# Performance work log

Hardware: AMD Instinct MI355X
Metric: run time of the kernel (lower is better)

Reference implementation:

```python
import jax, jax.numpy as jnp
import numpy as np

N_PTS, N_NODES, N_EDGES, N_CMP = 512, 10000, 50000, 64
# edge types produced by _get_edge_states, plus NULL (do_include_null=True, do_include_all_16=False)
EDGE_TYPES = jnp.array([0, 2, 3, 5, 9], dtype=jnp.int32)  # NULL, NOR, NCONV, NIMPL, AND
N_TYPES = 5
# mapping of temp = 2*a+b in {0,1,2,3} -> edge-type code
TEMP_TO_CODE = jnp.array([2, 3, 5, 9], dtype=jnp.int32)  # NOR, NCONV, NIMPL, AND


def _edge_to_logical(es):
    # es: (n, E) int codes -> (n, N_TYPES*E) bool, type-major layout matching
    # torch.permute([1,0,2]).reshape(n, n_types*n_edges)
    oh = es[:, None, :] == EDGE_TYPES[None, :, None]  # (n, N_TYPES, E)
    return oh.reshape(es.shape[0], N_TYPES * es.shape[1])


def setup_inputs() -> dict:
    key = jax.random.key(0)
    k1, k2, k3 = jax.random.split(key, 3)
    node_activations = jax.random.randint(k1, (N_PTS, N_NODES), 0, 2, dtype=jnp.int32)
    edge_endnode_idx = jax.random.randint(k2, (N_EDGES, 2), 0, N_NODES, dtype=jnp.int32)
    # learned edge states: random categorical over the 5 reachable types
    learned_type_idx = jax.random.randint(k3, (N_CMP, N_EDGES), 0, N_TYPES, dtype=jnp.int32)
    learned_codes = EDGE_TYPES[learned_type_idx]
    binarized_learned = _edge_to_logical(learned_codes).astype(jnp.float32)  # (N_CMP, 5*E)
    return {
        "node_activations": node_activations,
        "binarized_learned": binarized_learned,
        "edge_endnode_idx": edge_endnode_idx,
    }


def reference(node_activations, binarized_learned, edge_endnode_idx):
    # gather endpoint activations: (n_pts, n_edges)
    a = node_activations[:, edge_endnode_idx[:, 0]]
    b = node_activations[:, edge_endnode_idx[:, 1]]
    temp = 2 * a + b  # in {0,1,2,3}
    code = TEMP_TO_CODE[temp]  # edge_type_filter is empty -> no filtering
    # one-hot encode edge states: (n_pts, 5*n_edges)
    bact = _edge_to_logical(code).astype(binarized_learned.dtype)
    # energies: (n_pts, n_cmp); torch does int8 matmul of the same 0/1 values
    energies = jnp.einsum('ck,nk->nc', binarized_learned, bact)
    return energies - jnp.min(energies)
```

## Files before the change

kernel.cpp:

```cpp
#include <hip/hip_runtime.h>
#include <stdint.h>

#define N_PTS   512
#define N_NODES 10000
#define N_EDGES 50000
#define N_CMP   64
#define W64     784
#define EBITS   (W64 * 64)
#define LSTRIDE (N_CMP * W64)
#define NCHUNK  49
#define CW      16
#define TN      16
#define BST_ROW 10016
#define NB_BST  ((N_NODES + 255) / 256)
#define NBLK_L  (NCHUNK * N_CMP)

typedef unsigned long long u64;

__global__ void build_all(const int* __restrict__ act, const float* __restrict__ BL,
                          u64* __restrict__ Lp, uint16_t* __restrict__ bsT) {
    int bid = blockIdx.x;
    int t = threadIdx.x;
    if (bid < NBLK_L) {
        __shared__ uint16_t sh[256];
        int c = bid / NCHUNK, bx = bid % NCHUNK;
        int e0 = bx * 1024 + 4 * t;
        int nla = 0, nlb = 0, ntz = 0xF;
        if (e0 < N_EDGES) {
            const float* base = BL + (size_t)c * (5 * N_EDGES) + e0;
            float4 p0 = *(const float4*)(base);
            float4 p2 = *(const float4*)(base + 2 * N_EDGES);
            float4 p3 = *(const float4*)(base + 3 * N_EDGES);
            float4 p4 = *(const float4*)(base + 4 * N_EDGES);
            #define B_(f) ((f) != 0.f ? 1 : 0)
            nla = (B_(p3.x) | B_(p4.x)) | ((B_(p3.y) | B_(p4.y)) << 1)
                | ((B_(p3.z) | B_(p4.z)) << 2) | ((B_(p3.w) | B_(p4.w)) << 3);
            nlb = (B_(p2.x) | B_(p4.x)) | ((B_(p2.y) | B_(p4.y)) << 1)
                | ((B_(p2.z) | B_(p4.z)) << 2) | ((B_(p2.w) | B_(p4.w)) << 3);
            ntz = B_(p0.x) | (B_(p0.y) << 1) | (B_(p0.z) << 2) | (B_(p0.w) << 3);
            #undef B_
        }
        sh[t] = (uint16_t)(nla | (nlb << 4) | (ntz << 8));
        __syncthreads();
        if (t < 48) {
            int p = t >> 4, w = t & 15;
            const u64* v = (const u64*)sh + w * 4;
            u64 word = 0;
            #pragma unroll
            for (int i = 0; i < 4; ++i) {
                u64 x = v[i];
                #pragma unroll
                for (int kk = 0; kk < 4; ++kk)
                    word |= ((x >> (16 * kk + 4 * p)) & 0xFULL) << (4 * (i * 4 + kk));
            }
            Lp[(size_t)p * LSTRIDE + (size_t)c * W64 + bx * 16 + w] = word;
        }
    } else {
        int rem = bid - NBLK_L;
        int g = rem / NB_BST, nb = rem % NB_BST;
        int node = nb * 256 + t;
        if (node < N_NODES) {
            uint32_t m = 0;
            #pragma unroll
            for (int p = 0; p < TN; ++p)
                m |= (act[(size_t)(g * TN + p) * N_NODES + node] != 0 ? 1u : 0u) << p;
            bsT[(size_t)g * BST_ROW + node] = (uint16_t)m;
        }
    }
}

__global__ void __launch_bounds__(512, 6)
match_fused(const u64* __restrict__ Lp, const uint16_t* __restrict__ bsT,
            const int2* __restrict__ edges, uint32_t* __restrict__ part32) {
    __shared__ u64 Ll[3][CW][65];
    __shared__ uint16_t bsTl[BST_ROW];
    __shared__ int2 edgl[CW * 64];

    int chunk = blockIdx.x;
    int g = blockIdx.y;
    int t = threadIdx.x;
    int lane = t & 63;
    int wave = t >> 6;
    int cw0 = chunk * CW;

    {
        int w = t & 15;
        #pragma unroll
        for (int pass = 0; pass < 6; ++pass) {
            int r = pass * 32 + (t >> 4);
            int plane = r >> 6, c = r & 63;
            Ll[plane][w][c] = Lp[(size_t)plane * LSTRIDE + (size_t)c * W64 + cw0 + w];
        }
    }
    {
        const uint4* src = (const uint4*)(bsT + (size_t)g * BST_ROW);
        uint4* dst = (uint4*)bsTl;
        for (int idx = t; idx < BST_ROW / 8; idx += 512) dst[idx] = src[idx];
    }
    {
        int e = chunk * 1024 + t;
        edgl[t]       = edges[min(e, N_EDGES - 1)];
        edgl[t + 512] = edges[min(e + 512, N_EDGES - 1)];
    }
    __syncthreads();

    int cnt0 = 0, cnt1 = 0;
    #pragma unroll
    for (int w = 0; w < CW; ++w) {
        int2 cur = edgl[w * 64 + lane];
        uint32_t a16 = bsTl[cur.x];
        uint32_t b16 = bsTl[cur.y];
        u64 A0 = __ballot((a16 >> wave) & 1);
        u64 B0 = __ballot((b16 >> wave) & 1);
        u64 A1 = __ballot((a16 >> (wave + 8)) & 1);
        u64 B1 = __ballot((b16 >> (wave + 8)) & 1);
        u64 la = Ll[0][w][lane];
        u64 lb = Ll[1][w][lane];
        u64 tz = Ll[2][w][lane];
        cnt0 += __popcll(tz | (la ^ A0) | (lb ^ B0));
        cnt1 += __popcll(tz | (la ^ A1) | (lb ^ B1));
    }
    part32[(((size_t)chunk * 32 + g) * 8 + wave) * 64 + lane] =
        (uint32_t)cnt0 | ((uint32_t)cnt1 << 16);
}

__global__ void reduce1(const uint32_t* __restrict__ part32, int* __restrict__ energy,
                        int* __restrict__ blockmin) {
    int t = blockIdx.x * 256 + threadIdx.x;
    int c = t & 63, n = t >> 6;
    int g = n >> 4, p = n & 15;
    int wv = p & 7, hi = (p >> 3) * 16;
    int s = 0;
    #pragma unroll 7
    for (int ch = 0; ch < NCHUNK; ++ch)
        s += (part32[(((size_t)ch * 32 + g) * 8 + wv) * 64 + c] >> hi) & 0xFFFF;
    int e = EBITS - s;
    energy[t] = e;
    int m = e;
    for (int off = 32; off; off >>= 1) m = min(m, __shfl_down(m, off, 64));
    __shared__ int wm[4];
    if ((threadIdx.x & 63) == 0) wm[threadIdx.x >> 6] = m;
    __syncthreads();
    if (threadIdx.x == 0) blockmin[blockIdx.x] = min(min(wm[0], wm[1]), min(wm[2], wm[3]));
}

__global__ void subk(const int* __restrict__ energy, const int* __restrict__ blockmin,
                     float* __restrict__ out) {
    __shared__ int wm[4];
    __shared__ int ms;
    int t = threadIdx.x;
    int m = t < 128 ? blockmin[t] : 0x7fffffff;
    for (int off = 32; off; off >>= 1) m = min(m, __shfl_down(m, off, 64));
    if ((t & 63) == 0) wm[t >> 6] = m;
    __syncthreads();
    if (t == 0) ms = min(wm[0], wm[1]);
    __syncthreads();
    int mv = ms;
    int i = blockIdx.x * 256 + t;
    int4 e = ((const int4*)energy)[i];
    ((float4*)out)[i] = make_float4((float)(e.x - mv), (float)(e.y - mv),
                                    (float)(e.z - mv), (float)(e.w - mv));
}

extern "C" void kernel_launch(void* const* d_in, const int* in_sizes, int n_in,
                              void* d_out, int out_size, void* d_ws, size_t ws_size,
                              hipStream_t stream) {
    const int*   act   = (const int*)d_in[0];
    const float* BL    = (const float*)d_in[1];
    const int2*  edges = (const int2*)d_in[2];
    float* out = (float*)d_out;

    u64* Lp = (u64*)d_ws;
    uint16_t* bsT = (uint16_t*)(Lp + 3 * (size_t)LSTRIDE);
    uint32_t* part32 = (uint32_t*)(bsT + 32 * (size_t)BST_ROW);
    int* energy   = (int*)(part32 + (size_t)NCHUNK * N_PTS / 2 * N_CMP);
    int* blockmin = energy + N_PTS * N_CMP;

    build_all   <<<NBLK_L + (N_PTS / TN) * NB_BST, 256, 0, stream>>>(act, BL, Lp, bsT);
    match_fused <<<dim3(NCHUNK, N_PTS / TN), 512, 0, stream>>>(Lp, bsT, edges, part32);
    reduce1     <<<N_PTS * N_CMP / 256, 256, 0, stream>>>(part32, energy, blockmin);
    subk        <<<N_PTS * N_CMP / 1024, 256, 0, stream>>>(energy, blockmin, out);
}
```

Baseline: 41.67 us.

## Pack 32 points per group and keep edge indices in registers

Each point-group now covers 32 points packed into 32-bit masks instead of 16. Every match block therefore handles four point sets per edge lookup, which halves the grid's y-dimension and the number of times the learned bit-planes and edges are reloaded. Edge endpoints are loaded straight into registers instead of staging them through shared memory. The costs are a doubled shared-memory bsT tile (about 40KB), lower occupancy (launch bounds 4), more ballots per iteration, and fewer blocks to fill the GPU.

Result: slower. 44.04 us (+5.7%).

```diff
diff --git a/kernel.cpp b/kernel.cpp
--- a/kernel.cpp
+++ b/kernel.cpp
@@ -10,7 +10,8 @@
 #define LSTRIDE (N_CMP * W64)
 #define NCHUNK  49
 #define CW      16
-#define TN      16
+#define TN      32
+#define NGRP    (N_PTS / TN)
 #define BST_ROW 10016
 #define NB_BST  ((N_NODES + 255) / 256)
 #define NBLK_L  (NCHUNK * N_CMP)
@@ -18,7 +19,7 @@
 typedef unsigned long long u64;
 
 __global__ void build_all(const int* __restrict__ act, const float* __restrict__ BL,
-                          u64* __restrict__ Lp, uint16_t* __restrict__ bsT) {
+                          u64* __restrict__ Lp, uint32_t* __restrict__ bsT) {
     int bid = blockIdx.x;
     int t = threadIdx.x;
     if (bid < NBLK_L) {
@@ -64,17 +65,16 @@
             #pragma unroll
             for (int p = 0; p < TN; ++p)
                 m |= (act[(size_t)(g * TN + p) * N_NODES + node] != 0 ? 1u : 0u) << p;
-            bsT[(size_t)g * BST_ROW + node] = (uint16_t)m;
+            bsT[(size_t)g * BST_ROW + node] = m;
         }
     }
 }
 
-__global__ void __launch_bounds__(512, 6)
-match_fused(const u64* __restrict__ Lp, const uint16_t* __restrict__ bsT,
-            const int2* __restrict__ edges, uint32_t* __restrict__ part32) {
+__global__ void __launch_bounds__(512, 4)
+match_fused(const u64* __restrict__ Lp, const uint32_t* __restrict__ bsT,
+            const int2* __restrict__ edges, uint2* __restrict__ part) {
     __shared__ u64 Ll[3][CW][65];
-    __shared__ uint16_t bsTl[BST_ROW];
-    __shared__ int2 edgl[CW * 64];
+    __shared__ uint32_t bsTl[BST_ROW];
 
     int chunk = blockIdx.x;
     int g = blockIdx.y;
@@ -82,6 +82,12 @@
     int lane = t & 63;
     int wave = t >> 6;
     int cw0 = chunk * CW;
+
+    int2 ereg[CW];
+    int ebase = chunk * 1024 + lane;
+    #pragma unroll
+    for (int w = 0; w < CW; ++w)
+        ereg[w] = edges[min(ebase + w * 64, N_EDGES - 1)];
 
     {
         int w = t & 15;
@@ -95,45 +101,51 @@
     {
         const uint4* src = (const uint4*)(bsT + (size_t)g * BST_ROW);
         uint4* dst = (uint4*)bsTl;
-        for (int idx = t; idx < BST_ROW / 8; idx += 512) dst[idx] = src[idx];
-    }
-    {
-        int e = chunk * 1024 + t;
-        edgl[t]       = edges[min(e, N_EDGES - 1)];
-        edgl[t + 512] = edges[min(e + 512, N_EDGES - 1)];
+        for (int idx = t; idx < BST_ROW / 4; idx += 512) dst[idx] = src[idx];
     }
     __syncthreads();
 
-    int cnt0 = 0, cnt1 = 0;
+    int cnt0 = 0, cnt1 = 0, cnt2 = 0, cnt3 = 0;
     #pragma unroll
     for (int w = 0; w < CW; ++w) {
-        int2 cur = edgl[w * 64 + lane];
-        uint32_t a16 = bsTl[cur.x];
-        uint32_t b16 = bsTl[cur.y];
-        u64 A0 = __ballot((a16 >> wave) & 1);
-        u64 B0 = __ballot((b16 >> wave) & 1);
-        u64 A1 = __ballot((a16 >> (wave + 8)) & 1);
-        u64 B1 = __ballot((b16 >> (wave + 8)) & 1);
+        int2 cur = ereg[w];
+        uint32_t a = bsTl[cur.x];
+        uint32_t b = bsTl[cur.y];
+        u64 A0 = __ballot((a >> wave) & 1);
+        u64 B0 = __ballot((b >> wave) & 1);
+        u64 A1 = __ballot((a >> (wave + 8)) & 1);
+        u64 B1 = __ballot((b >> (wave + 8)) & 1);
+        u64 A2 = __ballot((a >> (wave + 16)) & 1);
+        u64 B2 = __ballot((b >> (wave + 16)) & 1);
+        u64 A3 = __ballot((a >> (wave + 24)) & 1);
+        u64 B3 = __ballot((b >> (wave + 24)) & 1);
         u64 la = Ll[0][w][lane];
         u64 lb = Ll[1][w][lane];
         u64 tz = Ll[2][w][lane];
         cnt0 += __popcll(tz | (la ^ A0) | (lb ^ B0));
         cnt1 += __popcll(tz | (la ^ A1) | (lb ^ B1));
+        cnt2 += __popcll(tz | (la ^ A2) | (lb ^ B2));
+        cnt3 += __popcll(tz | (la ^ A3) | (lb ^ B3));
     }
-    part32[(((size_t)chunk * 32 + g) * 8 + wave) * 64 + lane] =
-        (uint32_t)cnt0 | ((uint32_t)cnt1 << 16);
+    part[(((size_t)chunk * NGRP + g) * 8 + wave) * 64 + lane] =
+        make_uint2((uint32_t)cnt0 | ((uint32_t)cnt1 << 16),
+                   (uint32_t)cnt2 | ((uint32_t)cnt3 << 16));
 }
 
-__global__ void reduce1(const uint32_t* __restrict__ part32, int* __restrict__ energy,
+__global__ void reduce1(const uint2* __restrict__ part, int* __restrict__ energy,
                         int* __restrict__ blockmin) {
     int t = blockIdx.x * 256 + threadIdx.x;
     int c = t & 63, n = t >> 6;
-    int g = n >> 4, p = n & 15;
-    int wv = p & 7, hi = (p >> 3) * 16;
+    int g = n >> 5, p = n & 31;
+    int wv = p & 7, jj = p >> 3;
+    int sh = (jj & 1) * 16;
     int s = 0;
     #pragma unroll 7
-    for (int ch = 0; ch < NCHUNK; ++ch)
-        s += (part32[(((size_t)ch * 32 + g) * 8 + wv) * 64 + c] >> hi) & 0xFFFF;
+    for (int ch = 0; ch < NCHUNK; ++ch) {
+        uint2 v = part[(((size_t)ch * NGRP + g) * 8 + wv) * 64 + c];
+        uint32_t word = (jj < 2) ? v.x : v.y;
+        s += (word >> sh) & 0xFFFF;
+    }
     int e = EBITS - s;
     energy[t] = e;
     int m = e;
@@ -171,13 +183,13 @@
     float* out = (float*)d_out;
 
     u64* Lp = (u64*)d_ws;
-    uint16_t* bsT = (uint16_t*)(Lp + 3 * (size_t)LSTRIDE);
-    uint32_t* part32 = (uint32_t*)(bsT + 32 * (size_t)BST_ROW);
-    int* energy   = (int*)(part32 + (size_t)NCHUNK * N_PTS / 2 * N_CMP);
+    uint32_t* bsT = (uint32_t*)(Lp + 3 * (size_t)LSTRIDE);
+    uint2* part = (uint2*)(bsT + (size_t)NGRP * BST_ROW);
+    int* energy   = (int*)(part + (size_t)NCHUNK * NGRP * 8 * 64);
     int* blockmin = energy + N_PTS * N_CMP;
 
-    build_all   <<<NBLK_L + (N_PTS / TN) * NB_BST, 256, 0, stream>>>(act, BL, Lp, bsT);
-    match_fused <<<dim3(NCHUNK, N_PTS / TN), 512, 0, stream>>>(Lp, bsT, edges, part32);
-    reduce1     <<<N_PTS * N_CMP / 256, 256, 0, stream>>>(part32, energy, blockmin);
+    build_all   <<<NBLK_L + NGRP * NB_BST, 256, 0, stream>>>(act, BL, Lp, bsT);
+    match_fused <<<dim3(NCHUNK, NGRP), 512, 0, stream>>>(Lp, bsT, edges, part);
+    reduce1     <<<N_PTS * N_CMP / 256, 256, 0, stream>>>(part, energy, blockmin);
     subk        <<<N_PTS * N_CMP / 1024, 256, 0, stream>>>(energy, blockmin, out);
 }
```

## Split edge words across waves and reduce per-point counts in shared memory

Applied to the files above, without the earlier changes.

Changes the work split in match_fused. Each wave now handles 2 of the 16 edge words and all 16 points, where before every wave looped over all 16 words for 2 points. This cuts the per-wave edge gathers and bsTl lookups by a factor of eight, and edges are now read straight from global memory instead of being staged in shared memory. In exchange the kernel uses 16 ballots per word, 16 count registers per thread, an extra barrier and a shared-memory reduction across the 8 waves that reuses the bsTl buffer. reduce1 is updated to match the new part32 layout.

Result: faster. 40.77 us (-2.2%).

```diff
diff --git a/kernel.cpp b/kernel.cpp
--- a/kernel.cpp
+++ b/kernel.cpp
@@ -11,6 +11,7 @@
 #define NCHUNK  49
 #define CW      16
 #define TN      16
+#define NGRP    (N_PTS / TN)
 #define BST_ROW 10016
 #define NB_BST  ((N_NODES + 255) / 256)
 #define NBLK_L  (NCHUNK * N_CMP)
@@ -73,8 +74,7 @@
 match_fused(const u64* __restrict__ Lp, const uint16_t* __restrict__ bsT,
             const int2* __restrict__ edges, uint32_t* __restrict__ part32) {
     __shared__ u64 Ll[3][CW][65];
-    __shared__ uint16_t bsTl[BST_ROW];
-    __shared__ int2 edgl[CW * 64];
+    __shared__ __align__(16) uint16_t bsTl[BST_ROW];
 
     int chunk = blockIdx.x;
     int g = blockIdx.y;
@@ -97,31 +97,42 @@
         uint4* dst = (uint4*)bsTl;
         for (int idx = t; idx < BST_ROW / 8; idx += 512) dst[idx] = src[idx];
     }
-    {
-        int e = chunk * 1024 + t;
-        edgl[t]       = edges[min(e, N_EDGES - 1)];
-        edgl[t + 512] = edges[min(e + 512, N_EDGES - 1)];
-    }
     __syncthreads();
 
-    int cnt0 = 0, cnt1 = 0;
+    uint32_t cnt[TN];
     #pragma unroll
-    for (int w = 0; w < CW; ++w) {
-        int2 cur = edgl[w * 64 + lane];
+    for (int p = 0; p < TN; ++p) cnt[p] = 0;
+
+    #pragma unroll
+    for (int j = 0; j < 2; ++j) {
+        int w = wave * 2 + j;
+        int2 cur = edges[min(chunk * 1024 + w * 64 + lane, N_EDGES - 1)];
         uint32_t a16 = bsTl[cur.x];
         uint32_t b16 = bsTl[cur.y];
-        u64 A0 = __ballot((a16 >> wave) & 1);
-        u64 B0 = __ballot((b16 >> wave) & 1);
-        u64 A1 = __ballot((a16 >> (wave + 8)) & 1);
-        u64 B1 = __ballot((b16 >> (wave + 8)) & 1);
         u64 la = Ll[0][w][lane];
         u64 lb = Ll[1][w][lane];
         u64 tz = Ll[2][w][lane];
-        cnt0 += __popcll(tz | (la ^ A0) | (lb ^ B0));
-        cnt1 += __popcll(tz | (la ^ A1) | (lb ^ B1));
+        #pragma unroll
+        for (int p = 0; p < TN; ++p) {
+            u64 A = __ballot((a16 >> p) & 1);
+            u64 B = __ballot((b16 >> p) & 1);
+            cnt[p] += __popcll(tz | (la ^ A) | (lb ^ B));
+        }
     }
-    part32[(((size_t)chunk * 32 + g) * 8 + wave) * 64 + lane] =
-        (uint32_t)cnt0 | ((uint32_t)cnt1 << 16);
+
+    __syncthreads();
+    uint32_t (*red32)[8][64] = (uint32_t (*)[8][64])bsTl;
+    #pragma unroll
+    for (int q = 0; q < 8; ++q)
+        red32[wave][q][lane] = cnt[2 * q] | (cnt[2 * q + 1] << 16);
+    __syncthreads();
+    {
+        int q = t >> 6, c = t & 63;
+        uint32_t s = 0;
+        #pragma unroll
+        for (int wv = 0; wv < 8; ++wv) s += red32[wv][q][c];
+        part32[(((size_t)chunk * NGRP + g) * 8 + q) * 64 + c] = s;
+    }
 }
 
 __global__ void reduce1(const uint32_t* __restrict__ part32, int* __restrict__ energy,
@@ -129,11 +140,11 @@
     int t = blockIdx.x * 256 + threadIdx.x;
     int c = t & 63, n = t >> 6;
     int g = n >> 4, p = n & 15;
-    int wv = p & 7, hi = (p >> 3) * 16;
+    int q = p >> 1, hi = (p & 1) * 16;
     int s = 0;
     #pragma unroll 7
     for (int ch = 0; ch < NCHUNK; ++ch)
-        s += (part32[(((size_t)ch * 32 + g) * 8 + wv) * 64 + c] >> hi) & 0xFFFF;
+        s += (part32[(((size_t)ch * NGRP + g) * 8 + q) * 64 + c] >> hi) & 0xFFFF;
     int e = EBITS - s;
     energy[t] = e;
     int m = e;
@@ -172,12 +183,12 @@
 
     u64* Lp = (u64*)d_ws;
     uint16_t* bsT = (uint16_t*)(Lp + 3 * (size_t)LSTRIDE);
-    uint32_t* part32 = (uint32_t*)(bsT + 32 * (size_t)BST_ROW);
-    int* energy   = (int*)(part32 + (size_t)NCHUNK * N_PTS / 2 * N_CMP);
+    uint32_t* part32 = (uint32_t*)(bsT + (size_t)NGRP * BST_ROW);
+    int* energy   = (int*)(part32 + (size_t)NCHUNK * NGRP * 8 * 64);
     int* blockmin = energy + N_PTS * N_CMP;
 
-    build_all   <<<NBLK_L + (N_PTS / TN) * NB_BST, 256, 0, stream>>>(act, BL, Lp, bsT);
-    match_fused <<<dim3(NCHUNK, N_PTS / TN), 512, 0, stream>>>(Lp, bsT, edges, part32);
+    build_all   <<<NBLK_L + NGRP * NB_BST, 256, 0, stream>>>(act, BL, Lp, bsT);
+    match_fused <<<dim3(NCHUNK, NGRP), 512, 0, stream>>>(Lp, bsT, edges, part32);
     reduce1     <<<N_PTS * N_CMP / 256, 256, 0, stream>>>(part32, energy, blockmin);
     subk        <<<N_PTS * N_CMP / 1024, 256, 0, stream>>>(energy, blockmin, out);
 }
```
